# Performance work log

Measured on AMD Instinct MI355X. Metric: run time of the kernel, lower is better.

The kernel has to match this reference:

```python
import jax, jax.numpy as jnp
import numpy as np

N_QUBITS = 12
N_LAYERS = 6
BATCH = 256
INPUT_DIM = 256
OUT_DIM = 64
PI = float(np.pi)


def _ry_mat(a):
    # a: scalar or (B,) real angle -> (...,2,2) complex64 RY matrix
    c, s = jnp.cos(a * 0.5), jnp.sin(a * 0.5)
    return jnp.stack([jnp.stack([c, -s], -1), jnp.stack([s, c], -1)], -2).astype(jnp.complex64)


def _rz_mat(a):
    # diag(e^{-i a/2}, e^{+i a/2})
    em = jnp.exp(-0.5j * a.astype(jnp.complex64))
    ep = jnp.exp(0.5j * a.astype(jnp.complex64))
    z = jnp.zeros_like(em)
    return jnp.stack([jnp.stack([em, z], -1), jnp.stack([z, ep], -1)], -2)


def _apply_1q(state, U, w):
    # shared (2,2) gate on wire w; state: (B, 2, ..., 2)
    s = jnp.moveaxis(state, w + 1, -1)
    s = jnp.einsum('ij,b...j->b...i', U, s)
    return jnp.moveaxis(s, -1, w + 1)


def _apply_1q_batched(state, U, w):
    # per-sample (B,2,2) gate on wire w
    s = jnp.moveaxis(state, w + 1, -1)
    s = jnp.einsum('bij,b...j->b...i', U, s)
    return jnp.moveaxis(s, -1, w + 1)


def _cnot(state, c, t):
    s0 = jnp.take(state, 0, axis=c + 1)
    s1 = jnp.take(state, 1, axis=c + 1)
    t_ax = t + 1 if t < c else t  # target axis index after removing control axis
    s1 = jnp.flip(s1, axis=t_ax)
    return jnp.stack([s0, s1], axis=c + 1)


def _cz(state, c, t):
    idx = [slice(None)] * (N_QUBITS + 1)
    idx[c + 1] = 1
    idx[t + 1] = 1
    return state.at[tuple(idx)].multiply(-1.0)


def _run_circuit(xq, q_weights):
    # xq: (B, n_qubits) in [-1,1]; forward passes xq*pi, circuit multiplies by pi again
    B = xq.shape[0]
    enc = xq * (PI * PI)
    state = jnp.zeros((B, 2 ** N_QUBITS), jnp.complex64).at[:, 0].set(1.0)
    state = state.reshape((B,) + (2,) * N_QUBITS)
    for i in range(N_QUBITS):
        state = _apply_1q_batched(state, _ry_mat(enc[:, i]), i)
    w = q_weights.reshape(N_LAYERS, N_QUBITS, 3)
    for layer in range(N_LAYERS):
        for i in range(N_QUBITS):
            # PennyLane order: RZ(w0) then RY(w1) then RZ(w2) -> U = RZ2 @ RY1 @ RZ0
            U = _rz_mat(w[layer, i, 2]) @ _ry_mat(w[layer, i, 1]) @ _rz_mat(w[layer, i, 0])
            state = _apply_1q(state, U, i)
        for i in range(N_QUBITS):
            state = _cnot(state, i, (i + 1) % N_QUBITS)
        if layer % 2 == 0 and layer < N_LAYERS - 1:
            for i in range(N_QUBITS):
                state = _apply_1q_batched(state, _ry_mat(enc[:, i] * 0.5), i)
        if layer % 2 == 1:
            for i in range(0, N_QUBITS - 2, 2):
                state = _cz(state, i, i + 2)
    # PauliZ expectation on wires 0,1,2
    p = (state.real ** 2 + state.imag ** 2).reshape(B, 2, 2, 2, -1).sum(-1)  # (B,2,2,2)
    z0 = (p[:, 0] - p[:, 1]).sum((-1, -2))
    z1 = (p[:, :, 0] - p[:, :, 1]).sum((-1, -2))
    z2 = (p[:, :, :, 0] - p[:, :, :, 1]).sum((-1, -2))
    return jnp.stack([z0, z1, z2], -1)  # (B, 3) float32


def _layernorm(h, g, b, eps=1e-5):
    mu = h.mean(-1, keepdims=True)
    var = ((h - mu) ** 2).mean(-1, keepdims=True)
    return (h - mu) * jax.lax.rsqrt(var + eps) * g + b


def _forward(x, W1, b1, g_ln, b_ln, W2, b2, W3, b3, q_weights, W4, b4, W5, b5):
    gelu = lambda t: jax.nn.gelu(t, approximate=False)
    h = gelu(x @ W1.T + b1)
    h = _layernorm(h, g_ln, b_ln)
    h = gelu(h @ W2.T + b2)
    xq = jnp.tanh(h @ W3.T + b3)  # (B, n_qubits)
    q = _run_circuit(xq, q_weights)  # (B, 3)
    return gelu(q @ W4.T + b4) @ W5.T + b5  # (B, OUT_DIM)


def setup_inputs() -> dict:
    key = jax.random.key(0)
    ks = jax.random.split(key, 8)
    rn = lambda k, shape, s=0.05: (jax.random.normal(k, shape) * s).astype(jnp.float32)
    return {
        'x': jax.random.normal(ks[0], (BATCH, INPUT_DIM), jnp.float32),
        'W1': rn(ks[1], (128, INPUT_DIM)), 'b1': jnp.zeros(128, jnp.float32),
        'g_ln': jnp.ones(128, jnp.float32), 'b_ln': jnp.zeros(128, jnp.float32),
        'W2': rn(ks[2], (64, 128)), 'b2': jnp.zeros(64, jnp.float32),
        'W3': rn(ks[3], (N_QUBITS, 64)), 'b3': jnp.zeros(N_QUBITS, jnp.float32),
        'q_weights': (jax.random.normal(ks[4], (N_LAYERS * N_QUBITS * 3,)) * 0.1).astype(jnp.float32),
        'W4': rn(ks[5], (32, 3)), 'b4': jnp.zeros(32, jnp.float32),
        'W5': rn(ks[6], (OUT_DIM, 32)), 'b5': jnp.zeros(OUT_DIM, jnp.float32),
    }


def reference(x, W1, b1, g_ln, b_ln, W2, b2, W3, b3, q_weights, W4, b4, W5, b5):
    return _forward(x, W1, b1, g_ln, b_ln, W2, b2, W3, b3, q_weights, W4, b4, W5, b5)
```

## Files before the change

### kernel.cpp

```cpp
#include <hip/hip_runtime.h>
#include <math.h>

#define NQ   12
#define NL   6
#define BATCH 256
#define NT   1024
#define PI2  9.869604401089358f

__device__ __forceinline__ float geluf(float x) {
    return 0.5f * x * (1.0f + erff(x * 0.70710678118654752f));
}

__device__ __forceinline__ int Pad(int x) { return x + (x >> 4) + (x >> 8); }

__device__ __forceinline__ int sigma(int x) {
    return (x & 0xC3) | ((x & 0x3C) << 6) | ((x >> 6) & 0x3C);
}

__device__ __forceinline__ int gmap(int j) {
    return ((j ^ (j >> 1)) & 0x3FF)
         | ((((j >> 10) ^ (j >> 11) ^ j) & 1) << 10)
         | ((((j >> 11) ^ j) & 1) << 11);
}

__device__ __forceinline__ float2 cmul(float2 a, float2 b) {
    return make_float2(fmaf(a.x, b.x, -a.y * b.y), fmaf(a.x, b.y, a.y * b.x));
}
__device__ __forceinline__ float2 cadd(float2 a, float2 b) {
    return make_float2(a.x + b.x, a.y + b.y);
}
__device__ __forceinline__ float2 cscale(float2 a, float s) {
    return make_float2(a.x * s, a.y * s);
}

template<int CTRL>
__device__ __forceinline__ float2 dppx(float2 v) {
    int x = __builtin_amdgcn_update_dpp(0, __float_as_int(v.x), CTRL, 0xF, 0xF, true);
    int y = __builtin_amdgcn_update_dpp(0, __float_as_int(v.y), CTRL, 0xF, 0xF, true);
    return make_float2(__int_as_float(x), __int_as_float(y));
}
template<int OFF>
__device__ __forceinline__ float2 swzx(float2 v) {
    int x = __builtin_amdgcn_ds_swizzle(__float_as_int(v.x), OFF);
    int y = __builtin_amdgcn_ds_swizzle(__float_as_int(v.y), OFF);
    return make_float2(__int_as_float(x), __int_as_float(y));
}
__device__ __forceinline__ float2 shflx32(float2 v) {
    return make_float2(__shfl_xor(v.x, 32, 64), __shfl_xor(v.y, 32, 64));
}

__device__ __forceinline__ void gate_reg(float2* a, const float2* Ug, int bit) {
    const float2 u00 = Ug[0], u01 = Ug[1], u10 = Ug[2], u11 = Ug[3];
    #pragma unroll
    for (int m = 0; m < 4; m++) {
        if (m & bit) continue;
        float2 x0 = a[m], x1 = a[m | bit];
        a[m]       = cadd(cmul(u00, x0), cmul(u01, x1));
        a[m | bit] = cadd(cmul(u10, x0), cmul(u11, x1));
    }
}
template<int CTRL>
__device__ __forceinline__ void gate_dpp(float2* a, const float2* Ug, bool sel) {
    const float2 cA = sel ? Ug[3] : Ug[0];
    const float2 cB = sel ? Ug[2] : Ug[1];
    #pragma unroll
    for (int m = 0; m < 4; m++) {
        float2 v = dppx<CTRL>(a[m]);
        a[m] = cadd(cmul(cA, a[m]), cmul(cB, v));
    }
}
template<int OFF>
__device__ __forceinline__ void gate_swz(float2* a, const float2* Ug, bool sel) {
    const float2 cA = sel ? Ug[3] : Ug[0];
    const float2 cB = sel ? Ug[2] : Ug[1];
    #pragma unroll
    for (int m = 0; m < 4; m++) {
        float2 v = swzx<OFF>(a[m]);
        a[m] = cadd(cmul(cA, a[m]), cmul(cB, v));
    }
}
__device__ __forceinline__ void gate_shfl32(float2* a, const float2* Ug, bool sel) {
    const float2 cA = sel ? Ug[3] : Ug[0];
    const float2 cB = sel ? Ug[2] : Ug[1];
    #pragma unroll
    for (int m = 0; m < 4; m++) {
        float2 v = shflx32(a[m]);
        a[m] = cadd(cmul(cA, a[m]), cmul(cB, v));
    }
}

__global__ __launch_bounds__(NT)
void qpu_kernel(const float* __restrict__ x,   const float* __restrict__ W1, const float* __restrict__ b1,
                const float* __restrict__ g_ln, const float* __restrict__ b_ln,
                const float* __restrict__ W2,  const float* __restrict__ b2,
                const float* __restrict__ W3,  const float* __restrict__ b3,
                const float* __restrict__ qw,  const float* __restrict__ W4, const float* __restrict__ b4,
                const float* __restrict__ W5,  const float* __restrict__ b5,
                float* __restrict__ out)
{
    __shared__ float2 bufA[4368];
    __shared__ float2 bufB[4368];
    __shared__ float2 Um[NL * NQ * 4];
    __shared__ float  xs[256];
    __shared__ float  pr[128 * 9];
    __shared__ float  h1n[128];
    __shared__ float  h2s[64];
    __shared__ float  xqs[NQ];
    __shared__ float  musd[2];
    __shared__ float  qv[3];
    __shared__ float  h4s[32];
    __shared__ float  zred[16][3];

    const int t = threadIdx.x;
    const int b = blockIdx.x;

    if (t < 256) xs[t] = x[b * 256 + t];
    __syncthreads();

    {
        const int o = t >> 3, part = t & 7;
        const float4* w = (const float4*)(W1 + o * 256) + part * 8;
        const float*  xp = xs + part * 32;
        float a0 = 0.f, a1 = 0.f, a2 = 0.f, a3 = 0.f;
        #pragma unroll
        for (int k = 0; k < 8; k++) {
            float4 wv = w[k];
            a0 = fmaf(wv.x, xp[4 * k + 0], a0);
            a1 = fmaf(wv.y, xp[4 * k + 1], a1);
            a2 = fmaf(wv.z, xp[4 * k + 2], a2);
            a3 = fmaf(wv.w, xp[4 * k + 3], a3);
        }
        pr[o * 9 + part] = (a0 + a1) + (a2 + a3);
    }
    __syncthreads();
    if (t < 128) {
        float s = 0.f;
        #pragma unroll
        for (int k = 0; k < 8; k++) s += pr[t * 9 + k];
        h1n[t] = geluf(s + b1[t]);
    }
    __syncthreads();

    if (t < 64) {
        float v0 = h1n[t], v1 = h1n[t + 64];
        float s1 = v0 + v1;
        float s2 = fmaf(v0, v0, v1 * v1);
        #pragma unroll
        for (int off = 32; off > 0; off >>= 1) {
            s1 += __shfl_down(s1, off);
            s2 += __shfl_down(s2, off);
        }
        if (t == 0) {
            float mu  = s1 * (1.f / 128.f);
            float var = s2 * (1.f / 128.f) - mu * mu;
            musd[0] = mu;
            musd[1] = rsqrtf(var + 1e-5f);
        }
    }
    __syncthreads();
    if (t < 128) h1n[t] = (h1n[t] - musd[0]) * musd[1] * g_ln[t] + b_ln[t];
    __syncthreads();

    if (t < 512) {
        const int o = t >> 3, part = t & 7;
        const float4* w = (const float4*)(W2 + o * 128) + part * 4;
        const float*  hp = h1n + part * 16;
        float a0 = 0.f, a1 = 0.f, a2 = 0.f, a3 = 0.f;
        #pragma unroll
        for (int k = 0; k < 4; k++) {
            float4 wv = w[k];
            a0 = fmaf(wv.x, hp[4 * k + 0], a0);
            a1 = fmaf(wv.y, hp[4 * k + 1], a1);
            a2 = fmaf(wv.z, hp[4 * k + 2], a2);
            a3 = fmaf(wv.w, hp[4 * k + 3], a3);
        }
        pr[o * 9 + part] = (a0 + a1) + (a2 + a3);
    }
    __syncthreads();
    if (t < 64) {
        float s = 0.f;
        #pragma unroll
        for (int k = 0; k < 8; k++) s += pr[t * 9 + k];
        h2s[t] = geluf(s + b2[t]);
    }
    __syncthreads();

    if (t < 96) {
        const int o = t >> 3, part = t & 7;
        const float4* w = (const float4*)(W3 + o * 64) + part * 2;
        const float*  hp = h2s + part * 8;
        float4 w0 = w[0], w1 = w[1];
        float s = 0.f;
        s = fmaf(w0.x, hp[0], s); s = fmaf(w0.y, hp[1], s);
        s = fmaf(w0.z, hp[2], s); s = fmaf(w0.w, hp[3], s);
        s = fmaf(w1.x, hp[4], s); s = fmaf(w1.y, hp[5], s);
        s = fmaf(w1.z, hp[6], s); s = fmaf(w1.w, hp[7], s);
        pr[o * 9 + part] = s;
    }
    __syncthreads();
    if (t < NQ) {
        float s = 0.f;
        #pragma unroll
        for (int k = 0; k < 8; k++) s += pr[t * 9 + k];
        xqs[t] = tanhf(s + b3[t]);
    }
    __syncthreads();

    if (t < NL * NQ) {
        const int l = t / NQ;
        const int i = t % NQ;
        float a  = qw[t * 3 + 0];
        float bb = qw[t * 3 + 1];
        float c  = qw[t * 3 + 2];
        float sb, cb;   sincosf(0.5f * bb, &sb, &cb);
        float apc = 0.5f * (a + c), amc = 0.5f * (a - c);
        float sapc, capc; sincosf(apc, &sapc, &capc);
        float samc, camc; sincosf(amc, &samc, &camc);
        float2 u00 = make_float2( cb * capc, -cb * sapc);
        float2 u01 = make_float2(-sb * camc, -sb * samc);
        float2 u10 = make_float2( sb * camc, -sb * samc);
        float2 u11 = make_float2( cb * capc,  cb * sapc);

        float theta = 0.f;
        bool merge = false;
        if (l == 0)      { theta = xqs[i] * PI2;        merge = true; }
        else if (l & 1)  { theta = xqs[i] * PI2 * 0.5f; merge = true; }
        if (merge) {
            float sy, cy; sincosf(0.5f * theta, &sy, &cy);
            float2 m00 = cadd(cscale(u00,  cy), cscale(u01, sy));
            float2 m01 = cadd(cscale(u00, -sy), cscale(u01, cy));
            float2 m10 = cadd(cscale(u10,  cy), cscale(u11, sy));
            float2 m11 = cadd(cscale(u10, -sy), cscale(u11, cy));
            u00 = m00; u01 = m01; u10 = m10; u11 = m11;
        }
        Um[t * 4 + 0] = u00;
        Um[t * 4 + 1] = u01;
        Um[t * 4 + 2] = u10;
        Um[t * 4 + 3] = u11;
    }
    __syncthreads();

    float2 a[4];
    #pragma unroll
    for (int m = 0; m < 4; m++) {
        const int i = gmap(4 * t + m);
        float2 acc = (i & 1) ? Um[11 * 4 + 2] : Um[11 * 4 + 0];
        #pragma unroll
        for (int bb = 1; bb < 12; bb++) {
            const float2* Uq = &Um[(11 - bb) * 4];
            float2 f = ((i >> bb) & 1) ? Uq[2] : Uq[0];
            acc = cmul(acc, f);
        }
        a[m] = acc;
    }

    #pragma unroll 1
    for (int l = 1; l < NL; l++) {
        const float2* UL = &Um[l * NQ * 4];

        gate_reg(a, &UL[11 * 4], 1);
        gate_reg(a, &UL[10 * 4], 2);
        gate_dpp<0xB1>  (a, &UL[9 * 4], (t >> 0) & 1);
        gate_dpp<0x4E>  (a, &UL[8 * 4], (t >> 1) & 1);
        gate_swz<0x101F>(a, &UL[7 * 4], (t >> 2) & 1);
        gate_dpp<0x128> (a, &UL[6 * 4], (t >> 3) & 1);
        gate_swz<0x401F>(a, &UL[5 * 4], (t >> 4) & 1);
        gate_shfl32     (a, &UL[4 * 4], (t >> 5) & 1);

        {
            const int base = Pad(4 * t);
            #pragma unroll
            for (int m = 0; m < 4; m++) bufB[base + m] = a[m];
            __syncthreads();
            const int sb = Pad(sigma(4 * t));
            #pragma unroll
            for (int m = 0; m < 4; m++) a[m] = bufB[sb + m];
        }

        gate_dpp<0xB1>  (a, &UL[3 * 4], (t >> 0) & 1);
        gate_dpp<0x4E>  (a, &UL[2 * 4], (t >> 1) & 1);
        gate_swz<0x101F>(a, &UL[1 * 4], (t >> 2) & 1);
        gate_dpp<0x128> (a, &UL[0 * 4], (t >> 3) & 1);

        if (l < NL - 1) {
            const int sb = Pad(sigma(4 * t));
            #pragma unroll
            for (int m = 0; m < 4; m++) bufA[sb + m] = a[m];
            __syncthreads();
            const bool czl = (l == 1) || (l == 3);
            #pragma unroll
            for (int m = 0; m < 4; m++) {
                const int j = 4 * t + m;
                float2 v = bufA[Pad(gmap(j))];
                if (czl && (__popc(j & (j << 2) & 0xAA8) & 1)) { v.x = -v.x; v.y = -v.y; }
                a[m] = v;
            }
        }
    }

    float z0 = 0.f, z1 = 0.f, z2 = 0.f;
    #pragma unroll
    for (int m = 0; m < 4; m++) {
        const int j = sigma(4 * t + m);
        float p = fmaf(a[m].x, a[m].x, a[m].y * a[m].y);
        z0 += (__popc(j & 0x7FF) & 1) ? -p : p;
        z1 += (__popc(j & 0xC00) & 1) ? -p : p;
        z2 += (__popc(j & 0xE00) & 1) ? -p : p;
    }
    #pragma unroll
    for (int off = 32; off > 0; off >>= 1) {
        z0 += __shfl_down(z0, off);
        z1 += __shfl_down(z1, off);
        z2 += __shfl_down(z2, off);
    }
    if ((t & 63) == 0) {
        zred[t >> 6][0] = z0;
        zred[t >> 6][1] = z1;
        zred[t >> 6][2] = z2;
    }
    __syncthreads();
    if (t == 0) {
        float q0 = 0.f, q1 = 0.f, q2 = 0.f;
        #pragma unroll
        for (int w = 0; w < 16; w++) {
            q0 += zred[w][0]; q1 += zred[w][1]; q2 += zred[w][2];
        }
        qv[0] = q0; qv[1] = q1; qv[2] = q2;
    }
    __syncthreads();

    if (t < 32) {
        float h = b4[t];
        h = fmaf(qv[0], W4[t * 3 + 0], h);
        h = fmaf(qv[1], W4[t * 3 + 1], h);
        h = fmaf(qv[2], W4[t * 3 + 2], h);
        h4s[t] = geluf(h);
    }
    __syncthreads();
    if (t < 64) {
        float acc = b5[t];
        #pragma unroll
        for (int h = 0; h < 32; h++) acc = fmaf(h4s[h], W5[t * 32 + h], acc);
        out[b * 64 + t] = acc;
    }
}

extern "C" void kernel_launch(void* const* d_in, const int* in_sizes, int n_in,
                              void* d_out, int out_size, void* d_ws, size_t ws_size,
                              hipStream_t stream) {
    (void)in_sizes; (void)n_in; (void)d_ws; (void)ws_size; (void)out_size;
    const float* x    = (const float*)d_in[0];
    const float* W1   = (const float*)d_in[1];
    const float* b1   = (const float*)d_in[2];
    const float* g_ln = (const float*)d_in[3];
    const float* b_ln = (const float*)d_in[4];
    const float* W2   = (const float*)d_in[5];
    const float* b2   = (const float*)d_in[6];
    const float* W3   = (const float*)d_in[7];
    const float* b3   = (const float*)d_in[8];
    const float* qw   = (const float*)d_in[9];
    const float* W4   = (const float*)d_in[10];
    const float* b4   = (const float*)d_in[11];
    const float* W5   = (const float*)d_in[12];
    const float* b5   = (const float*)d_in[13];
    float* out = (float*)d_out;

    qpu_kernel<<<BATCH, NT, 0, stream>>>(x, W1, b1, g_ln, b_ln, W2, b2,
                                         W3, b3, qw, W4, b4, W5, b5, out);
}
```

Before: 105.8 us.

## Halve block to 512 threads with 8 amplitudes per thread and packed complex math

The state-vector simulation now uses 512 threads per sample, each holding 8 amplitudes instead of 4. Three qubits per phase are handled in registers and three via DPP, which removes the ds_swizzle and cross-half shuffle gates. Complex arithmetic moves to a 2-wide float vector type so the compiler can emit packed FMA instructions. The qubit-to-lane mapping, the initial product-state construction and the final Z-expectation reduction are reworked to match, and the MLP stages are re-split for fewer threads. The cost is more registers per thread and less parallelism per block.

```diff
diff --git a/kernel.cpp b/kernel.cpp
--- a/kernel.cpp
+++ b/kernel.cpp
@@ -4,18 +4,16 @@
 #define NQ   12
 #define NL   6
 #define BATCH 256
-#define NT   1024
+#define NT   512
 #define PI2  9.869604401089358f
+
+typedef float v2f __attribute__((ext_vector_type(2)));
 
 __device__ __forceinline__ float geluf(float x) {
     return 0.5f * x * (1.0f + erff(x * 0.70710678118654752f));
 }
 
 __device__ __forceinline__ int Pad(int x) { return x + (x >> 4) + (x >> 8); }
-
-__device__ __forceinline__ int sigma(int x) {
-    return (x & 0xC3) | ((x & 0x3C) << 6) | ((x >> 6) & 0x3C);
-}
 
 __device__ __forceinline__ int gmap(int j) {
     return ((j ^ (j >> 1)) & 0x3FF)
@@ -23,69 +21,40 @@
          | ((((j >> 11) ^ j) & 1) << 11);
 }
 
-__device__ __forceinline__ float2 cmul(float2 a, float2 b) {
-    return make_float2(fmaf(a.x, b.x, -a.y * b.y), fmaf(a.x, b.y, a.y * b.x));
-}
-__device__ __forceinline__ float2 cadd(float2 a, float2 b) {
-    return make_float2(a.x + b.x, a.y + b.y);
-}
-__device__ __forceinline__ float2 cscale(float2 a, float s) {
-    return make_float2(a.x * s, a.y * s);
+__device__ __forceinline__ v2f mk2(float a, float b) { v2f r; r.x = a; r.y = b; return r; }
+__device__ __forceinline__ v2f spl(float s)          { v2f r; r.x = s; r.y = s; return r; }
+__device__ __forceinline__ v2f swn(v2f x)            { v2f r; r.x = -x.y; r.y = x.x; return r; }
+__device__ __forceinline__ v2f cml(v2f u, v2f x)          { return spl(u.x) * x + spl(u.y) * swn(x); }
+__device__ __forceinline__ v2f cma(v2f u, v2f x, v2f acc) { return acc + spl(u.x) * x + spl(u.y) * swn(x); }
+
+__device__ __forceinline__ void bf(v2f& x0, v2f& x1, const v2f* U) {
+    v2f o0 = cma(U[1], x1, cml(U[0], x0));
+    v2f o1 = cma(U[3], x1, cml(U[2], x0));
+    x0 = o0; x1 = o1;
+}
+
+__device__ __forceinline__ void gate_reg(v2f* a, const v2f* U, int bit) {
+    #pragma unroll
+    for (int m = 0; m < 8; m++) {
+        if (m & bit) continue;
+        bf(a[m], a[m | bit], U);
+    }
 }
 
 template<int CTRL>
-__device__ __forceinline__ float2 dppx(float2 v) {
+__device__ __forceinline__ v2f dppv(v2f v) {
     int x = __builtin_amdgcn_update_dpp(0, __float_as_int(v.x), CTRL, 0xF, 0xF, true);
     int y = __builtin_amdgcn_update_dpp(0, __float_as_int(v.y), CTRL, 0xF, 0xF, true);
-    return make_float2(__int_as_float(x), __int_as_float(y));
-}
-template<int OFF>
-__device__ __forceinline__ float2 swzx(float2 v) {
-    int x = __builtin_amdgcn_ds_swizzle(__float_as_int(v.x), OFF);
-    int y = __builtin_amdgcn_ds_swizzle(__float_as_int(v.y), OFF);
-    return make_float2(__int_as_float(x), __int_as_float(y));
-}
-__device__ __forceinline__ float2 shflx32(float2 v) {
-    return make_float2(__shfl_xor(v.x, 32, 64), __shfl_xor(v.y, 32, 64));
-}
-
-__device__ __forceinline__ void gate_reg(float2* a, const float2* Ug, int bit) {
-    const float2 u00 = Ug[0], u01 = Ug[1], u10 = Ug[2], u11 = Ug[3];
+    return mk2(__int_as_float(x), __int_as_float(y));
+}
+template<int CTRL>
+__device__ __forceinline__ void gate_dpp(v2f* a, const v2f* U, bool sel) {
+    const v2f cA = sel ? U[3] : U[0];
+    const v2f cB = sel ? U[2] : U[1];
     #pragma unroll
-    for (int m = 0; m < 4; m++) {
-        if (m & bit) continue;
-        float2 x0 = a[m], x1 = a[m | bit];
-        a[m]       = cadd(cmul(u00, x0), cmul(u01, x1));
-        a[m | bit] = cadd(cmul(u10, x0), cmul(u11, x1));
-    }
-}
-template<int CTRL>
-__device__ __forceinline__ void gate_dpp(float2* a, const float2* Ug, bool sel) {
-    const float2 cA = sel ? Ug[3] : Ug[0];
-    const float2 cB = sel ? Ug[2] : Ug[1];
-    #pragma unroll
-    for (int m = 0; m < 4; m++) {
-        float2 v = dppx<CTRL>(a[m]);
-        a[m] = cadd(cmul(cA, a[m]), cmul(cB, v));
-    }
-}
-template<int OFF>
-__device__ __forceinline__ void gate_swz(float2* a, const float2* Ug, bool sel) {
-    const float2 cA = sel ? Ug[3] : Ug[0];
-    const float2 cB = sel ? Ug[2] : Ug[1];
-    #pragma unroll
-    for (int m = 0; m < 4; m++) {
-        float2 v = swzx<OFF>(a[m]);
-        a[m] = cadd(cmul(cA, a[m]), cmul(cB, v));
-    }
-}
-__device__ __forceinline__ void gate_shfl32(float2* a, const float2* Ug, bool sel) {
-    const float2 cA = sel ? Ug[3] : Ug[0];
-    const float2 cB = sel ? Ug[2] : Ug[1];
-    #pragma unroll
-    for (int m = 0; m < 4; m++) {
-        float2 v = shflx32(a[m]);
-        a[m] = cadd(cmul(cA, a[m]), cmul(cB, v));
+    for (int m = 0; m < 8; m++) {
+        v2f v = dppv<CTRL>(a[m]);
+        a[m] = cma(cB, v, cml(cA, a[m]));
     }
 }
 
@@ -98,18 +67,18 @@
                 const float* __restrict__ W5,  const float* __restrict__ b5,
                 float* __restrict__ out)
 {
-    __shared__ float2 bufA[4368];
-    __shared__ float2 bufB[4368];
-    __shared__ float2 Um[NL * NQ * 4];
-    __shared__ float  xs[256];
-    __shared__ float  pr[128 * 9];
-    __shared__ float  h1n[128];
-    __shared__ float  h2s[64];
-    __shared__ float  xqs[NQ];
-    __shared__ float  musd[2];
-    __shared__ float  qv[3];
-    __shared__ float  h4s[32];
-    __shared__ float  zred[16][3];
+    __shared__ v2f   bufA[4368];
+    __shared__ v2f   bufB[4368];
+    __shared__ v2f   Um[NL * NQ * 4];
+    __shared__ float xs[256];
+    __shared__ float pr[1280];
+    __shared__ float h1n[128];
+    __shared__ float h2s[64];
+    __shared__ float xqs[NQ];
+    __shared__ float musd[2];
+    __shared__ float qv[3];
+    __shared__ float h4s[32];
+    __shared__ float zred[8][3];
 
     const int t = threadIdx.x;
     const int b = blockIdx.x;
@@ -118,25 +87,23 @@
     __syncthreads();
 
     {
-        const int o = t >> 3, part = t & 7;
-        const float4* w = (const float4*)(W1 + o * 256) + part * 8;
-        const float*  xp = xs + part * 32;
+        const int o = t >> 2, part = t & 3;
+        const float4* w  = (const float4*)(W1 + o * 256) + part * 16;
+        const float*  xp = xs + part * 64;
         float a0 = 0.f, a1 = 0.f, a2 = 0.f, a3 = 0.f;
         #pragma unroll
-        for (int k = 0; k < 8; k++) {
+        for (int k = 0; k < 16; k++) {
             float4 wv = w[k];
             a0 = fmaf(wv.x, xp[4 * k + 0], a0);
             a1 = fmaf(wv.y, xp[4 * k + 1], a1);
             a2 = fmaf(wv.z, xp[4 * k + 2], a2);
             a3 = fmaf(wv.w, xp[4 * k + 3], a3);
         }
-        pr[o * 9 + part] = (a0 + a1) + (a2 + a3);
+        pr[o * 5 + part] = (a0 + a1) + (a2 + a3);
     }
     __syncthreads();
     if (t < 128) {
-        float s = 0.f;
-        #pragma unroll
-        for (int k = 0; k < 8; k++) s += pr[t * 9 + k];
+        float s = pr[t * 5 + 0] + pr[t * 5 + 1] + pr[t * 5 + 2] + pr[t * 5 + 3];
         h1n[t] = geluf(s + b1[t]);
     }
     __syncthreads();
@@ -161,20 +128,22 @@
     if (t < 128) h1n[t] = (h1n[t] - musd[0]) * musd[1] * g_ln[t] + b_ln[t];
     __syncthreads();
 
-    if (t < 512) {
+    {
         const int o = t >> 3, part = t & 7;
-        const float4* w = (const float4*)(W2 + o * 128) + part * 4;
-        const float*  hp = h1n + part * 16;
-        float a0 = 0.f, a1 = 0.f, a2 = 0.f, a3 = 0.f;
-        #pragma unroll
-        for (int k = 0; k < 4; k++) {
-            float4 wv = w[k];
-            a0 = fmaf(wv.x, hp[4 * k + 0], a0);
-            a1 = fmaf(wv.y, hp[4 * k + 1], a1);
-            a2 = fmaf(wv.z, hp[4 * k + 2], a2);
-            a3 = fmaf(wv.w, hp[4 * k + 3], a3);
-        }
-        pr[o * 9 + part] = (a0 + a1) + (a2 + a3);
+        if (o < 64) {
+            const float4* w  = (const float4*)(W2 + o * 128) + part * 4;
+            const float*  hp = h1n + part * 16;
+            float a0 = 0.f, a1 = 0.f, a2 = 0.f, a3 = 0.f;
+            #pragma unroll
+            for (int k = 0; k < 4; k++) {
+                float4 wv = w[k];
+                a0 = fmaf(wv.x, hp[4 * k + 0], a0);
+                a1 = fmaf(wv.y, hp[4 * k + 1], a1);
+                a2 = fmaf(wv.z, hp[4 * k + 2], a2);
+                a3 = fmaf(wv.w, hp[4 * k + 3], a3);
+            }
+            pr[o * 9 + part] = (a0 + a1) + (a2 + a3);
+        }
     }
     __syncthreads();
     if (t < 64) {
@@ -187,7 +156,7 @@
 
     if (t < 96) {
         const int o = t >> 3, part = t & 7;
-        const float4* w = (const float4*)(W3 + o * 64) + part * 2;
+        const float4* w  = (const float4*)(W3 + o * 64) + part * 2;
         const float*  hp = h2s + part * 8;
         float4 w0 = w[0], w1 = w[1];
         float s = 0.f;
@@ -216,10 +185,10 @@
         float apc = 0.5f * (a + c), amc = 0.5f * (a - c);
         float sapc, capc; sincosf(apc, &sapc, &capc);
         float samc, camc; sincosf(amc, &samc, &camc);
-        float2 u00 = make_float2( cb * capc, -cb * sapc);
-        float2 u01 = make_float2(-sb * camc, -sb * samc);
-        float2 u10 = make_float2( sb * camc, -sb * samc);
-        float2 u11 = make_float2( cb * capc,  cb * sapc);
+        float u00x =  cb * capc, u00y = -cb * sapc;
+        float u01x = -sb * camc, u01y = -sb * samc;
+        float u10x =  sb * camc, u10y = -sb * samc;
+        float u11x =  cb * capc, u11y =  cb * sapc;
 
         float theta = 0.f;
         bool merge = false;
@@ -227,86 +196,107 @@
         else if (l & 1)  { theta = xqs[i] * PI2 * 0.5f; merge = true; }
         if (merge) {
             float sy, cy; sincosf(0.5f * theta, &sy, &cy);
-            float2 m00 = cadd(cscale(u00,  cy), cscale(u01, sy));
-            float2 m01 = cadd(cscale(u00, -sy), cscale(u01, cy));
-            float2 m10 = cadd(cscale(u10,  cy), cscale(u11, sy));
-            float2 m11 = cadd(cscale(u10, -sy), cscale(u11, cy));
-            u00 = m00; u01 = m01; u10 = m10; u11 = m11;
-        }
-        Um[t * 4 + 0] = u00;
-        Um[t * 4 + 1] = u01;
-        Um[t * 4 + 2] = u10;
-        Um[t * 4 + 3] = u11;
-    }
-    __syncthreads();
-
-    float2 a[4];
-    #pragma unroll
-    for (int m = 0; m < 4; m++) {
-        const int i = gmap(4 * t + m);
-        float2 acc = (i & 1) ? Um[11 * 4 + 2] : Um[11 * 4 + 0];
-        #pragma unroll
-        for (int bb = 1; bb < 12; bb++) {
-            const float2* Uq = &Um[(11 - bb) * 4];
-            float2 f = ((i >> bb) & 1) ? Uq[2] : Uq[0];
-            acc = cmul(acc, f);
-        }
-        a[m] = acc;
-    }
-
+            float m00x = u00x * cy + u01x * sy, m00y = u00y * cy + u01y * sy;
+            float m01x = -u00x * sy + u01x * cy, m01y = -u00y * sy + u01y * cy;
+            float m10x = u10x * cy + u11x * sy, m10y = u10y * cy + u11y * sy;
+            float m11x = -u10x * sy + u11x * cy, m11y = -u10y * sy + u11y * cy;
+            u00x = m00x; u00y = m00y; u01x = m01x; u01y = m01y;
+            u10x = m10x; u10y = m10y; u11x = m11x; u11y = m11y;
+        }
+        Um[t * 4 + 0] = mk2(u00x, u00y);
+        Um[t * 4 + 1] = mk2(u01x, u01y);
+        Um[t * 4 + 2] = mk2(u10x, u10y);
+        Um[t * 4 + 3] = mk2(u11x, u11y);
+    }
+    __syncthreads();
+
+    const int PwA = 8 * t + (t >> 1) + (t >> 5);
+    const int s0  = (((t     ) & 1) << 9) | (((t >> 1) & 1) << 10) | ((t >> 2) & 1)
+                  | (((t >> 3) & 1) << 11) | (((t >> 4) & 1) << 1)  | (((t >> 5) & 1) << 2)
+                  | (((t >> 6) & 1) << 3)  | (((t >> 7) & 1) << 4)  | (((t >> 8) & 1) << 6);
+    const int Ps  = Pad(s0);
+    const int g8  = gmap(8 * t);
+
+    v2f a[8];
+    {
+        v2f common = Um[(11 - 3) * 4 + ((g8 >> 3) & 1) * 2];
+        #pragma unroll
+        for (int k = 4; k <= 9; k++) {
+            common = cml(common, Um[(11 - k) * 4 + ((g8 >> k) & 1) * 2]);
+        }
+        #pragma unroll
+        for (int m = 0; m < 8; m++) {
+            const int gmc = (m ^ (m >> 1)) | ((m & 1) ? 0xC00 : 0);
+            const int g = g8 ^ gmc;
+            v2f v = common;
+            v = cml(v, Um[11 * 4 + ((g     ) & 1) * 2]);
+            v = cml(v, Um[10 * 4 + ((g >> 1) & 1) * 2]);
+            v = cml(v, Um[ 9 * 4 + ((g >> 2) & 1) * 2]);
+            v = cml(v, Um[ 1 * 4 + ((g >> 10) & 1) * 2]);
+            v = cml(v, Um[ 0 * 4 + ((g >> 11) & 1) * 2]);
+            a[m] = v;
+        }
+    }
+
+    const bool d1 = t & 1, d2 = t & 2, d8 = t & 8;
     #pragma unroll 1
     for (int l = 1; l < NL; l++) {
-        const float2* UL = &Um[l * NQ * 4];
+        const v2f* UL = &Um[l * NQ * 4];
 
         gate_reg(a, &UL[11 * 4], 1);
         gate_reg(a, &UL[10 * 4], 2);
-        gate_dpp<0xB1>  (a, &UL[9 * 4], (t >> 0) & 1);
-        gate_dpp<0x4E>  (a, &UL[8 * 4], (t >> 1) & 1);
-        gate_swz<0x101F>(a, &UL[7 * 4], (t >> 2) & 1);
-        gate_dpp<0x128> (a, &UL[6 * 4], (t >> 3) & 1);
-        gate_swz<0x401F>(a, &UL[5 * 4], (t >> 4) & 1);
-        gate_shfl32     (a, &UL[4 * 4], (t >> 5) & 1);
-
-        {
-            const int base = Pad(4 * t);
+        gate_reg(a, &UL[ 9 * 4], 4);
+        gate_dpp<0xB1> (a, &UL[8 * 4], d1);
+        gate_dpp<0x4E> (a, &UL[7 * 4], d2);
+        gate_dpp<0x128>(a, &UL[5 * 4], d8);
+
+        #pragma unroll
+        for (int m = 0; m < 8; m++) bufB[PwA + m] = a[m];
+        __syncthreads();
+        #pragma unroll
+        for (int m = 0; m < 8; m++) {
+            const int dm = 34 * (m & 1) + 136 * ((m >> 1) & 1) + 273 * ((m >> 2) & 1);
+            a[m] = bufB[Ps + dm];
+        }
+
+        gate_reg(a, &UL[6 * 4], 1);
+        gate_reg(a, &UL[4 * 4], 2);
+        gate_reg(a, &UL[3 * 4], 4);
+        gate_dpp<0xB1> (a, &UL[2 * 4], d1);
+        gate_dpp<0x4E> (a, &UL[1 * 4], d2);
+        gate_dpp<0x128>(a, &UL[0 * 4], d8);
+
+        if (l < NL - 1) {
             #pragma unroll
-            for (int m = 0; m < 4; m++) bufB[base + m] = a[m];
-            __syncthreads();
-            const int sb = Pad(sigma(4 * t));
-            #pragma unroll
-            for (int m = 0; m < 4; m++) a[m] = bufB[sb + m];
-        }
-
-        gate_dpp<0xB1>  (a, &UL[3 * 4], (t >> 0) & 1);
-        gate_dpp<0x4E>  (a, &UL[2 * 4], (t >> 1) & 1);
-        gate_swz<0x101F>(a, &UL[1 * 4], (t >> 2) & 1);
-        gate_dpp<0x128> (a, &UL[0 * 4], (t >> 3) & 1);
-
-        if (l < NL - 1) {
-            const int sb = Pad(sigma(4 * t));
-            #pragma unroll
-            for (int m = 0; m < 4; m++) bufA[sb + m] = a[m];
+            for (int m = 0; m < 8; m++) {
+                const int dm = 34 * (m & 1) + 136 * ((m >> 1) & 1) + 273 * ((m >> 2) & 1);
+                bufA[Ps + dm] = a[m];
+            }
             __syncthreads();
             const bool czl = (l == 1) || (l == 3);
             #pragma unroll
-            for (int m = 0; m < 4; m++) {
-                const int j = 4 * t + m;
-                float2 v = bufA[Pad(gmap(j))];
-                if (czl && (__popc(j & (j << 2) & 0xAA8) & 1)) { v.x = -v.x; v.y = -v.y; }
+            for (int m = 0; m < 8; m++) {
+                const int gmc = (m ^ (m >> 1)) | ((m & 1) ? 0xC00 : 0);
+                const int g = g8 ^ gmc;
+                v2f v = bufA[Pad(g)];
+                const int j = 8 * t + m;
+                if (czl && (__popc(j & (j << 2) & 0xAA8) & 1)) v = -v;
                 a[m] = v;
             }
         }
     }
 
-    float z0 = 0.f, z1 = 0.f, z2 = 0.f;
+    float alt = 0.f, tot = 0.f;
     #pragma unroll
-    for (int m = 0; m < 4; m++) {
-        const int j = sigma(4 * t + m);
-        float p = fmaf(a[m].x, a[m].x, a[m].y * a[m].y);
-        z0 += (__popc(j & 0x7FF) & 1) ? -p : p;
-        z1 += (__popc(j & 0xC00) & 1) ? -p : p;
-        z2 += (__popc(j & 0xE00) & 1) ? -p : p;
-    }
+    for (int m = 0; m < 8; m++) {
+        float p = a[m].x * a[m].x + a[m].y * a[m].y;
+        tot += p;
+        alt += (__popc(m) & 1) ? -p : p;
+    }
+    float z0 = (__popc(t & 0x1F7) & 1) ? -alt : alt;
+    float z1 = (__popc(t & 0x00A) & 1) ? -tot : tot;
+    float z2 = (__popc(t & 0x00B) & 1) ? -tot : tot;
+
     #pragma unroll
     for (int off = 32; off > 0; off >>= 1) {
         z0 += __shfl_down(z0, off);
@@ -322,7 +312,7 @@
     if (t == 0) {
         float q0 = 0.f, q1 = 0.f, q2 = 0.f;
         #pragma unroll
-        for (int w = 0; w < 16; w++) {
+        for (int w = 0; w < 8; w++) {
             q0 += zred[w][0]; q1 += zred[w][1]; q2 += zred[w][2];
         }
         qv[0] = q0; qv[1] = q1; qv[2] = q2;
```

Measured after the change: 108.3 us. 2.4% more time.
